# Performance work log

Measured on AMD Instinct MI355X. Metric: run time of the kernel, lower is better.

The kernel has to match this reference:

```python
import jax, jax.numpy as jnp
import numpy as np

B, D_MODEL, C, T = 2, 256, 64, 1024
N_HEADS = 8
EPS = 1e-5


def setup_inputs() -> dict:
    key = jax.random.key(0)
    k1, k2, k3 = jax.random.split(key, 3)
    x = jax.random.normal(k1, (B, D_MODEL, C, T), dtype=jnp.float32)
    in_w = jax.random.normal(k2, (3 * D_MODEL, D_MODEL), dtype=jnp.float32) * 0.05
    in_b = jnp.zeros((3 * D_MODEL,), jnp.float32)
    out_w = jax.random.normal(k3, (D_MODEL, D_MODEL), dtype=jnp.float32) * 0.05
    out_b = jnp.zeros((D_MODEL,), jnp.float32)
    return dict(x=x, in_w=in_w, in_b=in_b, out_w=out_w, out_b=out_b)


def reference(x, in_w, in_b, out_w, out_b):
    b, d, c, t = x.shape
    h = N_HEADS
    f = d // h
    scale = 1.0 / np.sqrt(f).astype(np.float32)

    # InstanceNorm2d (no affine): normalize each (b, channel) over spatial (c, t)
    mu = x.mean(axis=(2, 3), keepdims=True)
    var = x.var(axis=(2, 3), keepdims=True)  # biased, as torch
    xn = (x - mu) / jnp.sqrt(var + EPS)

    # 1x1 conv d -> 3d
    qkv = jnp.einsum('bdct,ed->bect', xn, in_w) + in_b[None, :, None, None]
    q, k, v = jnp.split(qkv, 3, axis=1)

    def to_heads(u):
        # b (h f) c t -> (b c) h f t
        u = u.reshape(b, h, f, c, t)
        u = u.transpose(0, 3, 1, 2, 4)
        return u.reshape(b * c, h, f, t)

    q = jax.nn.softmax(to_heads(q), axis=-2) * scale  # softmax over feature dim
    k = jax.nn.softmax(to_heads(k), axis=-1)          # softmax over length dim
    v = to_heads(v) / t

    # context: [n, h, f_k, f_v]
    ctx = jnp.einsum('nhkl,nhvl->nhkv', k, v)
    out = jnp.einsum('nhdv,nhdl->nhvl', ctx, q)

    # (b c) h f t -> b (h f) c t
    out = out.reshape(b, c, h, f, t).transpose(0, 2, 3, 1, 4).reshape(b, d, c, t)

    out = jnp.einsum('bdct,ed->bect', out, out_w) + out_b[None, :, None, None]
    return out + x
```

## Files before the change

### kernel.cpp

```cpp
#include <hip/hip_runtime.h>
#include <stdint.h>

#define D_MODEL 256
#define TDIM    1024
#define NHEADS  8
#define FDIM    32
#define P_LEN   65536
#define K3      768
#define BK      64

using u16 = unsigned short;

typedef __bf16 bf16x8 __attribute__((ext_vector_type(8)));
typedef float  floatx4 __attribute__((ext_vector_type(4)));

__device__ __forceinline__ float b2f(u16 u) {
    union { float f; uint32_t i; } v; v.i = ((uint32_t)u) << 16; return v.f;
}
__device__ __forceinline__ float b2f_lo(uint32_t u) {
    union { float f; uint32_t i; } v; v.i = u << 16; return v.f;
}
__device__ __forceinline__ float b2f_hi(uint32_t u) {
    union { float f; uint32_t i; } v; v.i = u & 0xffff0000u; return v.f;
}
__device__ __forceinline__ u16 f2b(float f) {
    union { float f; uint32_t i; } v; v.f = f;
    uint32_t i = v.i;
    uint32_t r = i + 0x7fffu + ((i >> 16) & 1u);
    return (u16)(r >> 16);
}
__device__ __forceinline__ uint32_t pack2(float lo, float hi) {
    return ((uint32_t)f2b(hi) << 16) | (uint32_t)f2b(lo);
}

__device__ __forceinline__ void gload_lds16(const u16* g, u16* l) {
    __builtin_amdgcn_global_load_lds((const __attribute__((address_space(1))) void*)g,
                                     (__attribute__((address_space(3))) void*)l,
                                     16, 0, 0);
}

__device__ __forceinline__ void stc(u16* p, float v) { *p = f2b(v); }
__device__ __forceinline__ void stc(float* p, float v) { *p = v; }

__global__ __launch_bounds__(256) void transpose_x(const float* __restrict__ x,
                                                   u16* __restrict__ xt,
                                                   float* __restrict__ pscr,
                                                   float* __restrict__ qscr) {
    __shared__ float tile[64][65];
    int p0 = blockIdx.x * 64;
    int d0 = blockIdx.y * 64;
    int tid = threadIdx.x;
    int dr = tid >> 4;
    int pc = (tid & 15) * 4;
#pragma unroll
    for (int it = 0; it < 4; ++it) {
        int d = it * 16 + dr;
        float4 v = *(const float4*)&x[(size_t)(d0 + d) * P_LEN + p0 + pc];
        tile[pc + 0][d] = v.x;
        tile[pc + 1][d] = v.y;
        tile[pc + 2][d] = v.z;
        tile[pc + 3][d] = v.w;
        float s = v.x + v.y + v.z + v.w;
        float sq = v.x * v.x + v.y * v.y + v.z * v.z + v.w * v.w;
#pragma unroll
        for (int off = 8; off; off >>= 1) {
            s  += __shfl_down(s, off, 16);
            sq += __shfl_down(sq, off, 16);
        }
        if ((tid & 15) == 0) {
            pscr[(size_t)(d0 + d) * 1024 + blockIdx.x] = s;
            qscr[(size_t)(d0 + d) * 1024 + blockIdx.x] = sq;
        }
    }
    __syncthreads();
    int pr = tid >> 3;
    int dc = (tid & 7) * 8;
#pragma unroll
    for (int it = 0; it < 2; ++it) {
        int p = it * 32 + pr;
        ushort4 o0 = make_ushort4(f2b(tile[p][dc + 0]), f2b(tile[p][dc + 1]),
                                  f2b(tile[p][dc + 2]), f2b(tile[p][dc + 3]));
        ushort4 o1 = make_ushort4(f2b(tile[p][dc + 4]), f2b(tile[p][dc + 5]),
                                  f2b(tile[p][dc + 6]), f2b(tile[p][dc + 7]));
        u16* dst = xt + (size_t)(p0 + p) * D_MODEL + d0 + dc;
        *(ushort4*)dst = o0;
        *(ushort4*)(dst + 4) = o1;
    }
}

__global__ __launch_bounds__(64) void reduce_stats(const float* __restrict__ pscr,
                                                   const float* __restrict__ qscr,
                                                   float* __restrict__ mu,
                                                   float* __restrict__ rstd) {
    int d = blockIdx.x, t = threadIdx.x;
    const float4* ps = (const float4*)(pscr + (size_t)d * 1024);
    const float4* qs = (const float4*)(qscr + (size_t)d * 1024);
    float s = 0.f, q = 0.f;
#pragma unroll
    for (int i = 0; i < 4; ++i) {
        float4 a = ps[t + i * 64]; s += a.x + a.y + a.z + a.w;
        float4 b = qs[t + i * 64]; q += b.x + b.y + b.z + b.w;
    }
    for (int off = 32; off; off >>= 1) {
        s += __shfl_down(s, off);
        q += __shfl_down(q, off);
    }
    if (t == 0) {
        float m = s * (1.f / 65536.f);
        float var = q * (1.f / 65536.f) - m * m;
        mu[d] = m;
        rstd[d] = rsqrtf(var + 1e-5f);
    }
}

__global__ __launch_bounds__(256) void fold_kernel(const float* __restrict__ in_w,
                                                   const float* __restrict__ in_b,
                                                   const float* __restrict__ mu,
                                                   const float* __restrict__ rstd,
                                                   u16* __restrict__ Wp,
                                                   float* __restrict__ bprime) {
    int e = blockIdx.x;
    int d = threadIdx.x;
    float m = mu[d];
    float r = rstd[d];
    float w = in_w[e * D_MODEL + d];
    Wp[(size_t)e * D_MODEL + d] = f2b(w * r);
    float contrib = w * r * m;
    for (int off = 32; off; off >>= 1) contrib += __shfl_down(contrib, off);
    __shared__ float rr[4];
    if ((d & 63) == 0) rr[d >> 6] = contrib;
    __syncthreads();
    if (d == 0) bprime[e] = in_b[e] - (rr[0] + rr[1] + rr[2] + rr[3]);
}

template <bool RESID, bool PERC, bool QSM, typename OT>
__global__ __launch_bounds__(256) void mgemm(const u16* __restrict__ A,
                                             const u16* __restrict__ Bt,
                                             const float* __restrict__ bias,
                                             const float* __restrict__ resid,
                                             OT* __restrict__ Cout,
                                             u16* __restrict__ qout) {
    __shared__ __align__(16) u16 As[128 * BK];
    __shared__ __align__(16) u16 Bs[128 * BK];
    const int tid  = threadIdx.x;
    const int wave = tid >> 6;
    const int lane = tid & 63;
    const int m0 = blockIdx.y * 128;
    const int p0 = blockIdx.x * 128;
    const int mw = (wave >> 1) * 64;
    const int nw = (wave & 1) * 64;

    const u16* Ab = PERC ? A + ((size_t)(blockIdx.x >> 3) << 16) : A;

    floatx4 acc[4][4];
#pragma unroll
    for (int i = 0; i < 4; ++i)
#pragma unroll
        for (int j = 0; j < 4; ++j) acc[i][j] = (floatx4){0.f, 0.f, 0.f, 0.f};

    const int srow = lane >> 3;
    const int schunk = lane & 7;
    const int q  = lane >> 4;
    const int rl = lane & 15;

    for (int s = 0; s < 4; ++s) {
        const int k0 = s * BK;
#pragma unroll
        for (int j = 0; j < 4; ++j) {
            int rbase = wave * 32 + j * 8;
            int r = rbase + srow;
            int cg = schunk ^ (r & 7);
            gload_lds16(Ab + ((size_t)(m0 + r) << 8) + k0 + cg * 8, &As[rbase * BK]);
            gload_lds16(Bt + ((size_t)(p0 + r) << 8) + k0 + cg * 8, &Bs[rbase * BK]);
        }
        __syncthreads();
#pragma unroll
        for (int ks = 0; ks < 2; ++ks) {
            bf16x8 af[4], bf[4];
#pragma unroll
            for (int ti = 0; ti < 4; ++ti) {
                int r = mw + 16 * ti + rl;
                int cp = (ks * 4 + q) ^ (r & 7);
                af[ti] = *(const bf16x8*)&As[r * BK + cp * 8];
            }
#pragma unroll
            for (int tj = 0; tj < 4; ++tj) {
                int r = nw + 16 * tj + rl;
                int cp = (ks * 4 + q) ^ (r & 7);
                bf[tj] = *(const bf16x8*)&Bs[r * BK + cp * 8];
            }
#pragma unroll
            for (int ti = 0; ti < 4; ++ti)
#pragma unroll
                for (int tj = 0; tj < 4; ++tj)
                    acc[ti][tj] = __builtin_amdgcn_mfma_f32_16x16x32_bf16(
                        af[ti], bf[tj], acc[ti][tj], 0, 0, 0);
        }
        __syncthreads();
    }

    if (QSM && blockIdx.y < 2) {
        float den[2][4] = {{0.f, 0.f, 0.f, 0.f}, {0.f, 0.f, 0.f, 0.f}};
#pragma unroll
        for (int ti = 0; ti < 4; ++ti) {
#pragma unroll
            for (int i = 0; i < 4; ++i) {
                int e = m0 + mw + 16 * ti + 4 * q + i;
                float bv = bias[e];
#pragma unroll
                for (int tj = 0; tj < 4; ++tj) {
                    float ex = __expf(acc[ti][tj][i] + bv);
                    acc[ti][tj][i] = ex;
                    den[ti >> 1][tj] += ex;
                }
            }
        }
#pragma unroll
        for (int hh = 0; hh < 2; ++hh)
#pragma unroll
            for (int tj = 0; tj < 4; ++tj) {
                float dsum = den[hh][tj];
                dsum += __shfl_xor(dsum, 16);
                dsum += __shfl_xor(dsum, 32);
                den[hh][tj] = 1.f / dsum;
            }
#pragma unroll
        for (int tj = 0; tj < 4; ++tj) {
            size_t p = (size_t)(p0 + nw + 16 * tj + rl);
            u16* row = qout + p * D_MODEL + m0 + mw;
#pragma unroll
            for (int ti = 0; ti < 4; ++ti) {
                float inv = den[ti >> 1][tj];
                ushort4 o = make_ushort4(f2b(acc[ti][tj][0] * inv),
                                         f2b(acc[ti][tj][1] * inv),
                                         f2b(acc[ti][tj][2] * inv),
                                         f2b(acc[ti][tj][3] * inv));
                *(ushort4*)(row + 16 * ti + 4 * q) = o;
            }
        }
        return;
    }
#pragma unroll
    for (int ti = 0; ti < 4; ++ti) {
#pragma unroll
        for (int i = 0; i < 4; ++i) {
            int e = m0 + mw + 16 * ti + 4 * q + i;
            float bv = bias[e];
            size_t rowbase = (size_t)e * P_LEN + p0 + nw;
#pragma unroll
            for (int tj = 0; tj < 4; ++tj) {
                size_t addr = rowbase + 16 * tj + rl;
                float v = acc[ti][tj][i] + bv;
                if (RESID) v += resid[addr];
                stc(Cout + addr, v);
            }
        }
    }
}

__global__ __launch_bounds__(256) void ctx_kernel(const u16* __restrict__ qkv,
                                                  float* __restrict__ ctx) {
    int bid = blockIdx.x;
    int c = bid >> 3, h = bid & 7;
    int tid = threadIdx.x;
    size_t colbase = (size_t)c * TDIM;
    const u16* kb = qkv + (size_t)(D_MODEL + h * FDIM) * P_LEN + colbase;
    const u16* vb = qkv + (size_t)(2 * D_MODEL + h * FDIM) * P_LEN + colbase;

    __shared__ float kinv[32];
    __shared__ __align__(16) u16 ekt[32 * 264];
    __shared__ __align__(16) u16 vsb[32 * 264];

    {
        int row = tid >> 3, g = tid & 7;
        const u16* krow = kb + (size_t)row * P_LEN;
        float s = 0.f;
#pragma unroll
        for (int i = 0; i < 16; ++i) {
            uint4 u = *(const uint4*)(krow + g * 8 + i * 64);
            s += __expf(b2f_lo(u.x)) + __expf(b2f_hi(u.x))
               + __expf(b2f_lo(u.y)) + __expf(b2f_hi(u.y))
               + __expf(b2f_lo(u.z)) + __expf(b2f_hi(u.z))
               + __expf(b2f_lo(u.w)) + __expf(b2f_hi(u.w));
        }
        for (int off = 4; off; off >>= 1) s += __shfl_down(s, off, 8);
        if (g == 0) kinv[row] = 0.17677669529663687f / (s * 1024.f);
    }
    __syncthreads();

    const int lane = tid & 63;
    const int wave = tid >> 6;
    const int rl = lane & 15, q = lane >> 4;
    const int mi = wave >> 1, ni = wave & 1;
    const int o  = tid & 31;
    const int r8 = tid >> 5;
    floatx4 acc = {0.f, 0.f, 0.f, 0.f};

    for (int ch = 0; ch < 4; ++ch) {
        int t0 = ch * 256;
        if (ch) __syncthreads();
#pragma unroll
        for (int pass = 0; pass < 4; ++pass) {
            int r = pass * 8 + r8;
            float iv = kinv[r];
            uint4 u = *((const uint4*)(kb + (size_t)r * P_LEN + t0) + o);
            uint4 w = *((const uint4*)(vb + (size_t)r * P_LEN + t0) + o);
            uint4 E;
            E.x = pack2(__expf(b2f_lo(u.x)) * iv, __expf(b2f_hi(u.x)) * iv);
            E.y = pack2(__expf(b2f_lo(u.y)) * iv, __expf(b2f_hi(u.y)) * iv);
            E.z = pack2(__expf(b2f_lo(u.z)) * iv, __expf(b2f_hi(u.z)) * iv);
            E.w = pack2(__expf(b2f_lo(u.w)) * iv, __expf(b2f_hi(u.w)) * iv);
            *(uint4*)&ekt[r * 264 + o * 8] = E;
            *(uint4*)&vsb[r * 264 + o * 8] = w;
        }
        __syncthreads();
#pragma unroll
        for (int ks = 0; ks < 8; ++ks) {
            bf16x8 a  = *(const bf16x8*)&ekt[(16 * mi + rl) * 264 + ks * 32 + q * 8];
            bf16x8 bv = *(const bf16x8*)&vsb[(16 * ni + rl) * 264 + ks * 32 + q * 8];
            acc = __builtin_amdgcn_mfma_f32_16x16x32_bf16(a, bv, acc, 0, 0, 0);
        }
    }

    float* co = ctx + (size_t)bid * 1024;
#pragma unroll
    for (int i = 0; i < 4; ++i)
        co[(16 * mi + 4 * q + i) * 32 + 16 * ni + rl] = acc[i];
}

__global__ __launch_bounds__(256) void wfold_kernel(const float* __restrict__ w2,
                                                    const float* __restrict__ ctx,
                                                    u16* __restrict__ w2p) {
    __shared__ float cs[8192];
    int c = blockIdx.x;
    int tid = threadIdx.x;
    const float4* cb = (const float4*)(ctx + (size_t)c * 8192);
#pragma unroll
    for (int i = 0; i < 8; ++i)
        ((float4*)cs)[i * 256 + tid] = cb[i * 256 + tid];
    __syncthreads();
    int e = blockIdx.y * 128 + (tid >> 1);
    int hh = tid & 1;
    const float* wrow = w2 + (size_t)e * 256;
    u16* orow = w2p + ((size_t)c << 16) + (size_t)e * 256;
#pragma unroll
    for (int hi = 0; hi < 4; ++hi) {
        int h = hh * 4 + hi;
        float w[32];
#pragma unroll
        for (int v = 0; v < 8; ++v) {
            float4 t4 = *(const float4*)&wrow[h * 32 + v * 4];
            w[v * 4 + 0] = t4.x; w[v * 4 + 1] = t4.y;
            w[v * 4 + 2] = t4.z; w[v * 4 + 3] = t4.w;
        }
        const float* chp = cs + h * 1024;
#pragma unroll
        for (int kc = 0; kc < 4; ++kc) {
            union { u16 u[8]; uint4 v4; } pk;
#pragma unroll
            for (int ki = 0; ki < 8; ++ki) {
                const float* ck = chp + (kc * 8 + ki) * 32;
                float acc = 0.f;
#pragma unroll
                for (int v = 0; v < 32; v += 4) {
                    float4 c4 = *(const float4*)&ck[v];
                    acc += w[v] * c4.x + w[v + 1] * c4.y
                         + w[v + 2] * c4.z + w[v + 3] * c4.w;
                }
                pk.u[ki] = f2b(acc);
            }
            *(uint4*)(orow + h * 32 + kc * 8) = pk.v4;
        }
    }
}

extern "C" void kernel_launch(void* const* d_in, const int* in_sizes, int n_in,
                              void* d_out, int out_size, void* d_ws, size_t ws_size,
                              hipStream_t stream) {
    const float* x     = (const float*)d_in[0];
    const float* in_w  = (const float*)d_in[1];
    const float* in_b  = (const float*)d_in[2];
    const float* out_w = (const float*)d_in[3];
    const float* out_b = (const float*)d_in[4];
    float* out = (float*)d_out;

    char* ws = (char*)d_ws;
    float* mu     = (float*)(ws);
    float* rstd   = (float*)(ws + 1024);
    u16*   Wp     = (u16*)(ws + 4096);
    float* bprime = (float*)(ws + 790528);
    u16*   tbuf   = (u16*)(ws + 796672);
    float* ctxb   = (float*)(ws + 796672);
    u16*   w2p    = (u16*)(ws + 796672 + 2097152);
    u16*   qkvb   = (u16*)(ws + 34351104);
    float* pscr   = (float*)(ws + 132917248);
    float* qscr   = (float*)(ws + 133965824);

    for (int b = 0; b < 2; ++b) {
        const float* xb = x + (size_t)b * D_MODEL * P_LEN;
        transpose_x<<<dim3(1024, 4), 256, 0, stream>>>(xb, tbuf, pscr, qscr);
        reduce_stats<<<256, 64, 0, stream>>>(pscr, qscr, mu, rstd);
        fold_kernel<<<K3, 256, 0, stream>>>(in_w, in_b, mu, rstd,
                                            Wp + (size_t)b * K3 * D_MODEL,
                                            bprime + b * K3);
        mgemm<false, false, true, u16><<<dim3(512, 6), 256, 0, stream>>>(
            Wp + (size_t)b * K3 * D_MODEL, tbuf, bprime + b * K3, nullptr,
            qkvb, qkvb );
        ctx_kernel<<<512, 256, 0, stream>>>(qkvb, ctxb);
        wfold_kernel<<<dim3(64, 2), 256, 0, stream>>>(out_w, ctxb, w2p);
        mgemm<true, true, false, float><<<dim3(512, 2), 256, 0, stream>>>(
            w2p, qkvb , out_b, xb, out + (size_t)b * D_MODEL * P_LEN, nullptr);
    }
}
```

Before: 570.2 us.

## Batch both samples into single launches via gridDim.z and fuse ctx softmax sum

```diff
diff --git a/kernel.cpp b/kernel.cpp
--- a/kernel.cpp
+++ b/kernel.cpp
@@ -14,9 +14,6 @@
 typedef __bf16 bf16x8 __attribute__((ext_vector_type(8)));
 typedef float  floatx4 __attribute__((ext_vector_type(4)));
 
-__device__ __forceinline__ float b2f(u16 u) {
-    union { float f; uint32_t i; } v; v.i = ((uint32_t)u) << 16; return v.f;
-}
 __device__ __forceinline__ float b2f_lo(uint32_t u) {
     union { float f; uint32_t i; } v; v.i = u << 16; return v.f;
 }
@@ -42,10 +39,20 @@
 __device__ __forceinline__ void stc(u16* p, float v) { *p = f2b(v); }
 __device__ __forceinline__ void stc(float* p, float v) { *p = v; }
 
-__global__ __launch_bounds__(256) void transpose_x(const float* __restrict__ x,
-                                                   u16* __restrict__ xt,
-                                                   float* __restrict__ pscr,
-                                                   float* __restrict__ qscr) {
+__global__ __launch_bounds__(256) void transpose_x(const float* __restrict__ x0,
+                                                   const float* __restrict__ x1,
+                                                   u16* __restrict__ t0,
+                                                   u16* __restrict__ t1,
+                                                   float* __restrict__ ps0,
+                                                   float* __restrict__ ps1,
+                                                   float* __restrict__ qs0,
+                                                   float* __restrict__ qs1) {
+    const int z = blockIdx.z;
+    const float* x = z ? x1 : x0;
+    u16* xt = z ? t1 : t0;
+    float* pscr = z ? ps1 : ps0;
+    float* qscr = z ? qs1 : qs0;
+
     __shared__ float tile[64][65];
     int p0 = blockIdx.x * 64;
     int d0 = blockIdx.y * 64;
@@ -88,10 +95,16 @@
     }
 }
 
-__global__ __launch_bounds__(64) void reduce_stats(const float* __restrict__ pscr,
-                                                   const float* __restrict__ qscr,
+__global__ __launch_bounds__(64) void reduce_stats(const float* __restrict__ ps0,
+                                                   const float* __restrict__ ps1,
+                                                   const float* __restrict__ qs0,
+                                                   const float* __restrict__ qs1,
                                                    float* __restrict__ mu,
-                                                   float* __restrict__ rstd) {
+                                                   float* __restrict__ rstd,
+                                                   int b0) {
+    const int z = blockIdx.z;
+    const float* pscr = z ? ps1 : ps0;
+    const float* qscr = z ? qs1 : qs0;
     int d = blockIdx.x, t = threadIdx.x;
     const float4* ps = (const float4*)(pscr + (size_t)d * 1024);
     const float4* qs = (const float4*)(qscr + (size_t)d * 1024);
@@ -108,8 +121,8 @@
     if (t == 0) {
         float m = s * (1.f / 65536.f);
         float var = q * (1.f / 65536.f) - m * m;
-        mu[d] = m;
-        rstd[d] = rsqrtf(var + 1e-5f);
+        mu[(b0 + z) * 256 + d] = m;
+        rstd[(b0 + z) * 256 + d] = rsqrtf(var + 1e-5f);
     }
 }
 
@@ -118,28 +131,44 @@
                                                    const float* __restrict__ mu,
                                                    const float* __restrict__ rstd,
                                                    u16* __restrict__ Wp,
-                                                   float* __restrict__ bprime) {
+                                                   float* __restrict__ bprime,
+                                                   int b0) {
+    const int b = b0 + blockIdx.z;
     int e = blockIdx.x;
     int d = threadIdx.x;
-    float m = mu[d];
-    float r = rstd[d];
+    float m = mu[b * 256 + d];
+    float r = rstd[b * 256 + d];
     float w = in_w[e * D_MODEL + d];
-    Wp[(size_t)e * D_MODEL + d] = f2b(w * r);
+    Wp[((size_t)b * K3 + e) * D_MODEL + d] = f2b(w * r);
     float contrib = w * r * m;
     for (int off = 32; off; off >>= 1) contrib += __shfl_down(contrib, off);
     __shared__ float rr[4];
     if ((d & 63) == 0) rr[d >> 6] = contrib;
     __syncthreads();
-    if (d == 0) bprime[e] = in_b[e] - (rr[0] + rr[1] + rr[2] + rr[3]);
+    if (d == 0) bprime[b * K3 + e] = in_b[e] - (rr[0] + rr[1] + rr[2] + rr[3]);
 }
 
 template <bool RESID, bool PERC, bool QSM, typename OT>
-__global__ __launch_bounds__(256) void mgemm(const u16* __restrict__ A,
-                                             const u16* __restrict__ Bt,
-                                             const float* __restrict__ bias,
-                                             const float* __restrict__ resid,
-                                             OT* __restrict__ Cout,
-                                             u16* __restrict__ qout) {
+__global__ __launch_bounds__(256) void mgemm(const u16* __restrict__ A0,
+                                             const u16* __restrict__ A1,
+                                             const u16* __restrict__ B0,
+                                             const u16* __restrict__ B1,
+                                             const float* __restrict__ bias0,
+                                             const float* __restrict__ bias1,
+                                             const float* __restrict__ resid0,
+                                             const float* __restrict__ resid1,
+                                             OT* __restrict__ C0,
+                                             OT* __restrict__ C1,
+                                             u16* __restrict__ qo0,
+                                             u16* __restrict__ qo1) {
+    const int z = blockIdx.z;
+    const u16* A = z ? A1 : A0;
+    const u16* Bt = z ? B1 : B0;
+    const float* bias = z ? bias1 : bias0;
+    const float* resid = z ? resid1 : resid0;
+    OT* Cout = z ? C1 : C0;
+    u16* qout = z ? qo1 : qo0;
+
     __shared__ __align__(16) u16 As[128 * BK];
     __shared__ __align__(16) u16 Bs[128 * BK];
     const int tid  = threadIdx.x;
@@ -258,8 +287,14 @@
     }
 }
 
-__global__ __launch_bounds__(256) void ctx_kernel(const u16* __restrict__ qkv,
-                                                  float* __restrict__ ctx) {
+__global__ __launch_bounds__(256) void ctx_kernel(const u16* __restrict__ qk0,
+                                                  const u16* __restrict__ qk1,
+                                                  float* __restrict__ cx0,
+                                                  float* __restrict__ cx1) {
+    const int zz = blockIdx.z;
+    const u16* qkv = zz ? qk1 : qk0;
+    float* ctx = zz ? cx1 : cx0;
+
     int bid = blockIdx.x;
     int c = bid >> 3, h = bid & 7;
     int tid = threadIdx.x;
@@ -267,26 +302,9 @@
     const u16* kb = qkv + (size_t)(D_MODEL + h * FDIM) * P_LEN + colbase;
     const u16* vb = qkv + (size_t)(2 * D_MODEL + h * FDIM) * P_LEN + colbase;
 
-    __shared__ float kinv[32];
+    __shared__ float ssum[32];
     __shared__ __align__(16) u16 ekt[32 * 264];
     __shared__ __align__(16) u16 vsb[32 * 264];
-
-    {
-        int row = tid >> 3, g = tid & 7;
-        const u16* krow = kb + (size_t)row * P_LEN;
-        float s = 0.f;
-#pragma unroll
-        for (int i = 0; i < 16; ++i) {
-            uint4 u = *(const uint4*)(krow + g * 8 + i * 64);
-            s += __expf(b2f_lo(u.x)) + __expf(b2f_hi(u.x))
-               + __expf(b2f_lo(u.y)) + __expf(b2f_hi(u.y))
-               + __expf(b2f_lo(u.z)) + __expf(b2f_hi(u.z))
-               + __expf(b2f_lo(u.w)) + __expf(b2f_hi(u.w));
-        }
-        for (int off = 4; off; off >>= 1) s += __shfl_down(s, off, 8);
-        if (g == 0) kinv[row] = 0.17677669529663687f / (s * 1024.f);
-    }
-    __syncthreads();
 
     const int lane = tid & 63;
     const int wave = tid >> 6;
@@ -295,6 +313,7 @@
     const int o  = tid & 31;
     const int r8 = tid >> 5;
     floatx4 acc = {0.f, 0.f, 0.f, 0.f};
+    float psum[4] = {0.f, 0.f, 0.f, 0.f};
 
     for (int ch = 0; ch < 4; ++ch) {
         int t0 = ch * 256;
@@ -302,14 +321,18 @@
 #pragma unroll
         for (int pass = 0; pass < 4; ++pass) {
             int r = pass * 8 + r8;
-            float iv = kinv[r];
             uint4 u = *((const uint4*)(kb + (size_t)r * P_LEN + t0) + o);
             uint4 w = *((const uint4*)(vb + (size_t)r * P_LEN + t0) + o);
+            float e0 = __expf(b2f_lo(u.x)), e1 = __expf(b2f_hi(u.x));
+            float e2 = __expf(b2f_lo(u.y)), e3 = __expf(b2f_hi(u.y));
+            float e4 = __expf(b2f_lo(u.z)), e5 = __expf(b2f_hi(u.z));
+            float e6 = __expf(b2f_lo(u.w)), e7 = __expf(b2f_hi(u.w));
+            psum[pass] += (e0 + e1) + (e2 + e3) + (e4 + e5) + (e6 + e7);
             uint4 E;
-            E.x = pack2(__expf(b2f_lo(u.x)) * iv, __expf(b2f_hi(u.x)) * iv);
-            E.y = pack2(__expf(b2f_lo(u.y)) * iv, __expf(b2f_hi(u.y)) * iv);
-            E.z = pack2(__expf(b2f_lo(u.z)) * iv, __expf(b2f_hi(u.z)) * iv);
-            E.w = pack2(__expf(b2f_lo(u.w)) * iv, __expf(b2f_hi(u.w)) * iv);
+            E.x = pack2(e0, e1);
+            E.y = pack2(e2, e3);
+            E.z = pack2(e4, e5);
+            E.w = pack2(e6, e7);
             *(uint4*)&ekt[r * 264 + o * 8] = E;
             *(uint4*)&vsb[r * 264 + o * 8] = w;
         }
@@ -322,15 +345,32 @@
         }
     }
 
+#pragma unroll
+    for (int pass = 0; pass < 4; ++pass) {
+        float s = psum[pass];
+        for (int off = 16; off; off >>= 1) s += __shfl_down(s, off, 32);
+        if (o == 0) ssum[pass * 8 + r8] = s;
+    }
+    __syncthreads();
+
     float* co = ctx + (size_t)bid * 1024;
 #pragma unroll
-    for (int i = 0; i < 4; ++i)
-        co[(16 * mi + 4 * q + i) * 32 + 16 * ni + rl] = acc[i];
+    for (int i = 0; i < 4; ++i) {
+        int krow = 16 * mi + 4 * q + i;
+        float iv = 0.17677669529663687f / (ssum[krow] * 1024.f);
+        co[krow * 32 + 16 * ni + rl] = acc[i] * iv;
+    }
 }
 
 __global__ __launch_bounds__(256) void wfold_kernel(const float* __restrict__ w2,
-                                                    const float* __restrict__ ctx,
-                                                    u16* __restrict__ w2p) {
+                                                    const float* __restrict__ cx0,
+                                                    const float* __restrict__ cx1,
+                                                    u16* __restrict__ wp0,
+                                                    u16* __restrict__ wp1) {
+    const int z = blockIdx.z;
+    const float* ctx = z ? cx1 : cx0;
+    u16* w2p = z ? wp1 : wp0;
+
     __shared__ float cs[8192];
     int c = blockIdx.x;
     int tid = threadIdx.x;
@@ -386,29 +426,58 @@
 
     char* ws = (char*)d_ws;
     float* mu     = (float*)(ws);
-    float* rstd   = (float*)(ws + 1024);
+    float* rstd   = (float*)(ws + 2048);
     u16*   Wp     = (u16*)(ws + 4096);
     float* bprime = (float*)(ws + 790528);
-    u16*   tbuf   = (u16*)(ws + 796672);
-    float* ctxb   = (float*)(ws + 796672);
-    u16*   w2p    = (u16*)(ws + 796672 + 2097152);
-    u16*   qkvb   = (u16*)(ws + 34351104);
-    float* pscr   = (float*)(ws + 132917248);
-    float* qscr   = (float*)(ws + 133965824);
-
-    for (int b = 0; b < 2; ++b) {
-        const float* xb = x + (size_t)b * D_MODEL * P_LEN;
-        transpose_x<<<dim3(1024, 4), 256, 0, stream>>>(xb, tbuf, pscr, qscr);
-        reduce_stats<<<256, 64, 0, stream>>>(pscr, qscr, mu, rstd);
-        fold_kernel<<<K3, 256, 0, stream>>>(in_w, in_b, mu, rstd,
-                                            Wp + (size_t)b * K3 * D_MODEL,
-                                            bprime + b * K3);
-        mgemm<false, false, true, u16><<<dim3(512, 6), 256, 0, stream>>>(
-            Wp + (size_t)b * K3 * D_MODEL, tbuf, bprime + b * K3, nullptr,
-            qkvb, qkvb );
-        ctx_kernel<<<512, 256, 0, stream>>>(qkvb, ctxb);
-        wfold_kernel<<<dim3(64, 2), 256, 0, stream>>>(out_w, ctxb, w2p);
-        mgemm<true, true, false, float><<<dim3(512, 2), 256, 0, stream>>>(
-            w2p, qkvb , out_b, xb, out + (size_t)b * D_MODEL * P_LEN, nullptr);
-    }
-}
+
+    const size_t NEED_BIG = 269232128;
+
+    auto chain = [&](int b0, int nb, u16* tb0, u16* tb1, u16* qk0, u16* qk1) {
+        int b1r = b0 + nb - 1;
+        const float* xb0 = x + (size_t)b0 * D_MODEL * P_LEN;
+        const float* xb1 = x + (size_t)b1r * D_MODEL * P_LEN;
+        float* ob0 = out + (size_t)b0 * D_MODEL * P_LEN;
+        float* ob1 = out + (size_t)b1r * D_MODEL * P_LEN;
+        float* ps0 = (float*)((char*)qk0 + 98566144);
+        float* ps1 = (float*)((char*)qk1 + 98566144);
+        float* qs0 = (float*)((char*)qk0 + 99614720);
+        float* qs1 = (float*)((char*)qk1 + 99614720);
+        float* cx0 = (float*)tb0;
+        float* cx1 = (float*)tb1;
+        u16* wp0 = (u16*)((char*)tb0 + 2097152);
+        u16* wp1 = (u16*)((char*)tb1 + 2097152);
+        const u16* A0 = Wp + (size_t)b0 * K3 * D_MODEL;
+        const u16* A1 = Wp + (size_t)b1r * K3 * D_MODEL;
+        const float* bb0 = bprime + b0 * K3;
+        const float* bb1 = bprime + b1r * K3;
+
+        transpose_x<<<dim3(1024, 4, nb), 256, 0, stream>>>(
+            xb0, xb1, tb0, tb1, ps0, ps1, qs0, qs1);
+        reduce_stats<<<dim3(256, 1, nb), 64, 0, stream>>>(
+            ps0, ps1, qs0, qs1, mu, rstd, b0);
+        fold_kernel<<<dim3(K3, 1, nb), 256, 0, stream>>>(
+            in_w, in_b, mu, rstd, Wp, bprime, b0);
+        mgemm<false, false, true, u16><<<dim3(512, 6, nb), 256, 0, stream>>>(
+            A0, A1, tb0, tb1, bb0, bb1, nullptr, nullptr,
+            qk0, qk1, qk0, qk1);
+        ctx_kernel<<<dim3(512, 1, nb), 256, 0, stream>>>(qk0, qk1, cx0, cx1);
+        wfold_kernel<<<dim3(64, 2, nb), 256, 0, stream>>>(
+            out_w, cx0, cx1, wp0, wp1);
+        mgemm<true, true, false, float><<<dim3(512, 2, nb), 256, 0, stream>>>(
+            wp0, wp1, qk0, qk1, out_b, out_b, xb0, xb1,
+            ob0, ob1, nullptr, nullptr);
+    };
+
+    if (ws_size >= NEED_BIG) {
+        u16* tb0 = (u16*)(ws + 796672);
+        u16* tb1 = (u16*)(ws + 34351104);
+        u16* qk0 = (u16*)(ws + 67905536);
+        u16* qk1 = (u16*)(ws + 168568832);
+        chain(0, 2, tb0, tb1, qk0, qk1);
+    } else {
+        u16* tb = (u16*)(ws + 796672);
+        u16* qk = (u16*)(ws + 34351104);
+        chain(0, 1, tb, tb, qk, qk);
+        chain(1, 1, tb, tb, qk, qk);
+    }
+}
```

New measurement: 632.5 us. +10.9%, slower.

## Remap GEMM blocks for XCD-aware locality and fuse key softmax sum into ctx pass

Applied to the files above, without the earlier changes.

```diff
diff --git a/kernel.cpp b/kernel.cpp
--- a/kernel.cpp
+++ b/kernel.cpp
@@ -14,9 +14,6 @@
 typedef __bf16 bf16x8 __attribute__((ext_vector_type(8)));
 typedef float  floatx4 __attribute__((ext_vector_type(4)));
 
-__device__ __forceinline__ float b2f(u16 u) {
-    union { float f; uint32_t i; } v; v.i = ((uint32_t)u) << 16; return v.f;
-}
 __device__ __forceinline__ float b2f_lo(uint32_t u) {
     union { float f; uint32_t i; } v; v.i = u << 16; return v.f;
 }
@@ -133,7 +130,7 @@
     if (d == 0) bprime[e] = in_b[e] - (rr[0] + rr[1] + rr[2] + rr[3]);
 }
 
-template <bool RESID, bool PERC, bool QSM, typename OT>
+template <bool RESID, bool PERC, bool QSM, int YT, typename OT>
 __global__ __launch_bounds__(256) void mgemm(const u16* __restrict__ A,
                                              const u16* __restrict__ Bt,
                                              const float* __restrict__ bias,
@@ -145,12 +142,19 @@
     const int tid  = threadIdx.x;
     const int wave = tid >> 6;
     const int lane = tid & 63;
-    const int m0 = blockIdx.y * 128;
-    const int p0 = blockIdx.x * 128;
+
+    const int bid = blockIdx.x;
+    const int per = (int)gridDim.x >> 3;
+    const int lid = (bid & 7) * per + (bid >> 3);
+    const int yy = lid % YT;
+    const int xx = lid / YT;
+
+    const int m0 = yy * 128;
+    const int p0 = xx * 128;
     const int mw = (wave >> 1) * 64;
     const int nw = (wave & 1) * 64;
 
-    const u16* Ab = PERC ? A + ((size_t)(blockIdx.x >> 3) << 16) : A;
+    const u16* Ab = PERC ? A + ((size_t)(xx >> 3) << 16) : A;
 
     floatx4 acc[4][4];
 #pragma unroll
@@ -199,7 +203,7 @@
         __syncthreads();
     }
 
-    if (QSM && blockIdx.y < 2) {
+    if (QSM && yy < 2) {
         float den[2][4] = {{0.f, 0.f, 0.f, 0.f}, {0.f, 0.f, 0.f, 0.f}};
 #pragma unroll
         for (int ti = 0; ti < 4; ++ti) {
@@ -267,26 +271,9 @@
     const u16* kb = qkv + (size_t)(D_MODEL + h * FDIM) * P_LEN + colbase;
     const u16* vb = qkv + (size_t)(2 * D_MODEL + h * FDIM) * P_LEN + colbase;
 
-    __shared__ float kinv[32];
+    __shared__ float ssum[32];
     __shared__ __align__(16) u16 ekt[32 * 264];
     __shared__ __align__(16) u16 vsb[32 * 264];
-
-    {
-        int row = tid >> 3, g = tid & 7;
-        const u16* krow = kb + (size_t)row * P_LEN;
-        float s = 0.f;
-#pragma unroll
-        for (int i = 0; i < 16; ++i) {
-            uint4 u = *(const uint4*)(krow + g * 8 + i * 64);
-            s += __expf(b2f_lo(u.x)) + __expf(b2f_hi(u.x))
-               + __expf(b2f_lo(u.y)) + __expf(b2f_hi(u.y))
-               + __expf(b2f_lo(u.z)) + __expf(b2f_hi(u.z))
-               + __expf(b2f_lo(u.w)) + __expf(b2f_hi(u.w));
-        }
-        for (int off = 4; off; off >>= 1) s += __shfl_down(s, off, 8);
-        if (g == 0) kinv[row] = 0.17677669529663687f / (s * 1024.f);
-    }
-    __syncthreads();
 
     const int lane = tid & 63;
     const int wave = tid >> 6;
@@ -295,6 +282,7 @@
     const int o  = tid & 31;
     const int r8 = tid >> 5;
     floatx4 acc = {0.f, 0.f, 0.f, 0.f};
+    float psum[4] = {0.f, 0.f, 0.f, 0.f};
 
     for (int ch = 0; ch < 4; ++ch) {
         int t0 = ch * 256;
@@ -302,14 +290,18 @@
 #pragma unroll
         for (int pass = 0; pass < 4; ++pass) {
             int r = pass * 8 + r8;
-            float iv = kinv[r];
             uint4 u = *((const uint4*)(kb + (size_t)r * P_LEN + t0) + o);
             uint4 w = *((const uint4*)(vb + (size_t)r * P_LEN + t0) + o);
+            float e0 = __expf(b2f_lo(u.x)), e1 = __expf(b2f_hi(u.x));
+            float e2 = __expf(b2f_lo(u.y)), e3 = __expf(b2f_hi(u.y));
+            float e4 = __expf(b2f_lo(u.z)), e5 = __expf(b2f_hi(u.z));
+            float e6 = __expf(b2f_lo(u.w)), e7 = __expf(b2f_hi(u.w));
+            psum[pass] += (e0 + e1) + (e2 + e3) + (e4 + e5) + (e6 + e7);
             uint4 E;
-            E.x = pack2(__expf(b2f_lo(u.x)) * iv, __expf(b2f_hi(u.x)) * iv);
-            E.y = pack2(__expf(b2f_lo(u.y)) * iv, __expf(b2f_hi(u.y)) * iv);
-            E.z = pack2(__expf(b2f_lo(u.z)) * iv, __expf(b2f_hi(u.z)) * iv);
-            E.w = pack2(__expf(b2f_lo(u.w)) * iv, __expf(b2f_hi(u.w)) * iv);
+            E.x = pack2(e0, e1);
+            E.y = pack2(e2, e3);
+            E.z = pack2(e4, e5);
+            E.w = pack2(e6, e7);
             *(uint4*)&ekt[r * 264 + o * 8] = E;
             *(uint4*)&vsb[r * 264 + o * 8] = w;
         }
@@ -322,10 +314,21 @@
         }
     }
 
+#pragma unroll
+    for (int pass = 0; pass < 4; ++pass) {
+        float s = psum[pass];
+        for (int off = 16; off; off >>= 1) s += __shfl_down(s, off, 32);
+        if (o == 0) ssum[pass * 8 + r8] = s;
+    }
+    __syncthreads();
+
     float* co = ctx + (size_t)bid * 1024;
 #pragma unroll
-    for (int i = 0; i < 4; ++i)
-        co[(16 * mi + 4 * q + i) * 32 + 16 * ni + rl] = acc[i];
+    for (int i = 0; i < 4; ++i) {
+        int krow = 16 * mi + 4 * q + i;
+        float iv = 0.17677669529663687f / (ssum[krow] * 1024.f);
+        co[krow * 32 + 16 * ni + rl] = acc[i] * iv;
+    }
 }
 
 __global__ __launch_bounds__(256) void wfold_kernel(const float* __restrict__ w2,
@@ -403,12 +406,13 @@
         fold_kernel<<<K3, 256, 0, stream>>>(in_w, in_b, mu, rstd,
                                             Wp + (size_t)b * K3 * D_MODEL,
                                             bprime + b * K3);
-        mgemm<false, false, true, u16><<<dim3(512, 6), 256, 0, stream>>>(
+        mgemm<false, false, true, 6, u16><<<3072, 256, 0, stream>>>(
             Wp + (size_t)b * K3 * D_MODEL, tbuf, bprime + b * K3, nullptr,
             qkvb, qkvb );
         ctx_kernel<<<512, 256, 0, stream>>>(qkvb, ctxb);
         wfold_kernel<<<dim3(64, 2), 256, 0, stream>>>(out_w, ctxb, w2p);
-        mgemm<true, true, false, float><<<dim3(512, 2), 256, 0, stream>>>(
-            w2p, qkvb , out_b, xb, out + (size_t)b * D_MODEL * P_LEN, nullptr);
-    }
-}
+        mgemm<true, true, false, 2, float><<<1024, 256, 0, stream>>>(
+            w2p, qkvb , out_b, xb, out + (size_t)b * D_MODEL * P_LEN,
+            nullptr);
+    }
+}
```

After: 671.6 us. 1.18x slower.
